# Kernel optimization log

Hardware: AMD Instinct MI355X
Metric: run time of the kernel (lower is better)

Reference implementation:

```python
import jax, jax.numpy as jnp
import numpy as np

B, T, C = 8, 2048, 1024
NEG_BIG = -1e30  # exp(NEG_BIG - row_max) underflows to exactly 0 in fp32


def setup_inputs() -> dict:
    key = jax.random.key(0)
    k1, k2 = jax.random.split(key)
    x = jax.random.normal(k1, (B, T, C), dtype=jnp.float32)
    # nn.Linear weight, shape [out, in]; forward computes x @ W^T
    W_H = jax.random.normal(k2, (C, C), dtype=jnp.float32) * (1.0 / np.sqrt(C))
    return {"x": x, "W_H": W_H}


def reference(x, W_H):
    Tdim = x.shape[1]
    xH = jnp.einsum('btc,dc->btd', x, W_H)          # H(x) = x @ W^T, [B,T,C]
    scores = jnp.einsum('btc,bsc->bts', x, xH)       # bilinear scores, [B,T,T]
    # tril_plus_one=True -> strictly-lower-triangular mask (diagonal=-1)
    mask = jnp.tril(jnp.ones((Tdim, Tdim), dtype=bool), k=-1)
    scores = jnp.where(mask, scores, NEG_BIG)
    wei = jax.nn.softmax(scores, axis=-1)            # fully-masked rows -> uniform, zeroed below
    all_masked = ~mask.any(axis=-1)                  # [T], True for row 0
    wei = jnp.where(all_masked[None, :, None], 0.0, wei)
    out = jnp.einsum('bts,bsc->btc', wei, xH)
    return -out
```

## Files before the change

### kernel.cpp

```cpp
#include <hip/hip_runtime.h>
#include <stdint.h>

#define Bn 8
#define Tn 2048
#define Cn 1024
#define Mn (Bn * Tn)
#define NTRI 136

typedef __attribute__((ext_vector_type(4))) float f32x4;
typedef _Float16 f16;
typedef __attribute__((ext_vector_type(8))) _Float16 f16x8;
typedef uint16_t u16;
typedef uint32_t u32;

static __device__ __forceinline__ u16 f2h(float f) {
  union { f16 h; u16 u; } c; c.h = (f16)f; return c.u;
}
static __device__ __forceinline__ f32x4 mfmaH(f16x8 a, f16x8 b, f32x4 c) {
  return __builtin_amdgcn_mfma_f32_16x16x32_f16(a, b, c, 0, 0, 0);
}
static __device__ __forceinline__ void gld16(const void* g, void* l) {
  __builtin_amdgcn_global_load_lds(
      (const __attribute__((address_space(1))) u32*)g,
      (__attribute__((address_space(3))) u32*)l, 16, 0, 0);
}

__global__ __launch_bounds__(256) void ksplitW(const float* __restrict__ s,
                                               u16* __restrict__ hi) {
  size_t i = ((size_t)blockIdx.x * 256 + threadIdx.x) * 8;
  float4 a = *(const float4*)(s + i), b = *(const float4*)(s + i + 4);
  float f[8] = {a.x, a.y, a.z, a.w, b.x, b.y, b.z, b.w};
  union { u16 u[8]; uint4 v; } H;
#pragma unroll
  for (int j = 0; j < 8; ++j) H.u[j] = f2h(f[j]);
  *(uint4*)(hi + i) = H.v;
}

__global__ __launch_bounds__(256) void ksplitX(const float* __restrict__ s,
                                               u16* __restrict__ hi,
                                               u16* __restrict__ lo) {
  size_t i = ((size_t)blockIdx.x * 256 + threadIdx.x) * 8;
  float4 a = *(const float4*)(s + i), b = *(const float4*)(s + i + 4);
  float f[8] = {a.x, a.y, a.z, a.w, b.x, b.y, b.z, b.w};
  union { u16 u[8]; uint4 v; } H, L;
#pragma unroll
  for (int j = 0; j < 8; ++j) {
    f16 h = (f16)f[j];
    union { f16 h; u16 u; } ch; ch.h = h;
    H.u[j] = ch.u;
    L.u[j] = f2h(f[j] - (float)h);
  }
  *(uint4*)(hi + i) = H.v;
  *(uint4*)(lo + i) = L.v;
}

__global__ __launch_bounds__(256) void k1_xh(const u16* __restrict__ x_h,
                                             const u16* __restrict__ W_h,
                                             u16* __restrict__ xh) {
  __shared__ __align__(16) u16 Ah[8192], Bh[8192];
  const int tid = threadIdx.x;
  const int m0 = blockIdx.x * 128, n0 = blockIdx.y * 128;
  const int wave = tid >> 6, lane = tid & 63;
  const int wrow = (wave >> 1) * 64, wcol = (wave & 1) * 64;
  const int quad = lane >> 4, l16 = lane & 15;

  f32x4 acc[4][4] = {};

  for (int k0 = 0; k0 < Cn; k0 += 64) {
#pragma unroll
    for (int i = 0; i < 4; ++i) {
      int chunk = i * 256 + tid;
      int kk = chunk >> 9, row = (chunk >> 2) & 127, c8 = (chunk & 3) * 8;
      gld16(x_h + (size_t)(m0 + row) * Cn + k0 + kk * 32 + c8, Ah + chunk * 8);
      gld16(W_h + (size_t)(n0 + row) * Cn + k0 + kk * 32 + c8, Bh + chunk * 8);
    }
    __syncthreads();
#pragma unroll
    for (int kk = 0; kk < 2; ++kk) {
      f16x8 a[4], b[4];
#pragma unroll
      for (int i = 0; i < 4; ++i) {
        a[i] = *(const f16x8*)(Ah + kk * 4096 + (wrow + i * 16 + l16) * 32 + quad * 8);
        b[i] = *(const f16x8*)(Bh + kk * 4096 + (wcol + i * 16 + l16) * 32 + quad * 8);
      }
#pragma unroll
      for (int mi = 0; mi < 4; ++mi)
#pragma unroll
        for (int ni = 0; ni < 4; ++ni)
          acc[mi][ni] = mfmaH(a[mi], b[ni], acc[mi][ni]);
    }
    __syncthreads();
  }
#pragma unroll
  for (int mi = 0; mi < 4; ++mi)
#pragma unroll
    for (int ni = 0; ni < 4; ++ni)
#pragma unroll
      for (int r = 0; r < 4; ++r) {
        int row = wrow + mi * 16 + quad * 4 + r;
        int col = wcol + ni * 16 + l16;
        xh[(size_t)(m0 + row) * Cn + n0 + col] = f2h(acc[mi][ni][r]);
      }
}

__global__ __launch_bounds__(512) void k2_scores(const u16* __restrict__ x_h,
                                                 const u16* __restrict__ x_l,
                                                 const u16* __restrict__ xh,
                                                 u16* __restrict__ P,
                                                 float* __restrict__ mt,
                                                 float* __restrict__ lt) {
  __shared__ __align__(16) union {
    struct { u16 Ah[2][4096], Al[2][4096], Bh[2][8192]; } s;
    struct { float Mrow[4][128]; float Lrow[4][128]; } e;
  } u;
  const int tid = threadIdx.x;

  const int bid = blockIdx.x;
  const int half = gridDim.x / 144;
  const int xcd = bid & 7, slot = bid >> 3;
  const int p = xcd & 3, h = xcd >> 2;
  const int n1 = 16 - 2 * p, n2 = 2 * p + 2;
  int c, j, bb;
  if (slot < n1 * half) {
    c = p; bb = slot / n1; j = slot % n1;
  } else {
    int s2 = slot - n1 * half; c = 7 - p; bb = s2 / n2; j = s2 % n2;
  }
  const int bL = h * half + bb;
  const int qt = 2 * c + j, bcol = c;
  const int t0 = qt * 128, s0 = bcol * 256;

  const int wave = tid >> 6, lane = tid & 63;
  const int wc = wave & 3;
  const int wrow = (wave >> 2) * 64, wcol = wc * 64;
  const int quad = lane >> 4, l16 = lane & 15;

  f32x4 acc[4][4] = {};
  const size_t abase = ((size_t)bL * Tn + t0) * Cn;
  const size_t bbase = ((size_t)bL * Tn + s0) * Cn;
  const int arow = tid >> 2, ac8 = (tid & 3) * 8;

  auto stage = [&](int buf, int k0) {
    size_t aoff = abase + (size_t)arow * Cn + k0 + ac8;
    gld16(x_h + aoff, &u.s.Ah[buf][tid * 8]);
    gld16(x_l + aoff, &u.s.Al[buf][tid * 8]);
#pragma unroll
    for (int i = 0; i < 2; ++i) {
      int ch = i * 512 + tid;
      int row = ch >> 2, c8 = (ch & 3) * 8;
      gld16(xh + bbase + (size_t)row * Cn + k0 + c8, &u.s.Bh[buf][ch * 8]);
    }
  };

  stage(0, 0);
  stage(1, 32);
#pragma unroll 1
  for (int kidx = 0; kidx < 32; ++kidx) {
    if (kidx < 31) {
      asm volatile("s_waitcnt vmcnt(4)" ::: "memory");
    } else {
      asm volatile("s_waitcnt vmcnt(0)" ::: "memory");
    }
    __builtin_amdgcn_s_barrier();
    __builtin_amdgcn_sched_barrier(0);
    const int cur = kidx & 1;
    f16x8 b[4];
#pragma unroll
    for (int ni = 0; ni < 4; ++ni)
      b[ni] = *(const f16x8*)&u.s.Bh[cur][(wcol + ni * 16 + l16) * 32 + quad * 8];
#pragma unroll
    for (int mi = 0; mi < 4; ++mi) {
      f16x8 ah = *(const f16x8*)&u.s.Ah[cur][(wrow + mi * 16 + l16) * 32 + quad * 8];
      f16x8 al = *(const f16x8*)&u.s.Al[cur][(wrow + mi * 16 + l16) * 32 + quad * 8];
#pragma unroll
      for (int ni = 0; ni < 4; ++ni) {
        acc[mi][ni] = mfmaH(ah, b[ni], acc[mi][ni]);
        acc[mi][ni] = mfmaH(al, b[ni], acc[mi][ni]);
      }
    }
    asm volatile("s_waitcnt lgkmcnt(0)" ::: "memory");
    __builtin_amdgcn_sched_barrier(0);
    __builtin_amdgcn_s_barrier();
    if (kidx < 30) stage(cur, (kidx + 2) * 32);
  }

  float rm[4][4];
#pragma unroll
  for (int mi = 0; mi < 4; ++mi)
#pragma unroll
    for (int r = 0; r < 4; ++r) {
      int row = wrow + mi * 16 + quad * 4 + r;
      float m = -1e30f;
#pragma unroll
      for (int ni = 0; ni < 4; ++ni) {
        int scol = s0 + wcol + ni * 16 + l16;
        if (scol >= t0 + row) acc[mi][ni][r] = -1e30f;
        m = fmaxf(m, acc[mi][ni][r]);
      }
      m = fmaxf(m, __shfl_xor(m, 1));
      m = fmaxf(m, __shfl_xor(m, 2));
      m = fmaxf(m, __shfl_xor(m, 4));
      m = fmaxf(m, __shfl_xor(m, 8));
      rm[mi][r] = m;
    }
  if (l16 == 0) {
#pragma unroll
    for (int mi = 0; mi < 4; ++mi)
#pragma unroll
      for (int r = 0; r < 4; ++r)
        u.e.Mrow[wc][wrow + mi * 16 + quad * 4 + r] = rm[mi][r];
  }
  __syncthreads();
  const int h2 = (wc >> 1) * 2;
  float rs[4][4];
#pragma unroll
  for (int mi = 0; mi < 4; ++mi)
#pragma unroll
    for (int r = 0; r < 4; ++r) {
      int row = wrow + mi * 16 + quad * 4 + r;
      float m2 = fmaxf(u.e.Mrow[h2][row], u.e.Mrow[h2 + 1][row]);
      float s = 0.f;
#pragma unroll
      for (int ni = 0; ni < 4; ++ni) {
        int scol = s0 + wcol + ni * 16 + l16;
        float pv = (scol < t0 + row) ? __expf(acc[mi][ni][r] - m2) : 0.0f;
        acc[mi][ni][r] = pv;
        s += pv;
      }
      s += __shfl_xor(s, 1);
      s += __shfl_xor(s, 2);
      s += __shfl_xor(s, 4);
      s += __shfl_xor(s, 8);
      rs[mi][r] = s;
      rm[mi][r] = m2;
    }
  if (l16 == 0) {
#pragma unroll
    for (int mi = 0; mi < 4; ++mi)
#pragma unroll
      for (int r = 0; r < 4; ++r)
        u.e.Lrow[wc][wrow + mi * 16 + quad * 4 + r] = rs[mi][r];
  }
  __syncthreads();
  const int st128 = bcol * 2 + (wc >> 1);
  if (st128 <= qt) {
    if ((wc & 1) == 0 && l16 == 0) {
#pragma unroll
      for (int mi = 0; mi < 4; ++mi)
#pragma unroll
        for (int r = 0; r < 4; ++r) {
          int row = wrow + mi * 16 + quad * 4 + r;
          size_t rI = (size_t)bL * Tn + t0 + row;
          mt[rI * 16 + st128] = rm[mi][r];
          lt[rI * 16 + st128] = u.e.Lrow[wc][row] + u.e.Lrow[wc + 1][row];
        }
    }
    const size_t pbase = (size_t)(bL * NTRI + qt * (qt + 1) / 2 + st128) * 16384;
#pragma unroll
    for (int mi = 0; mi < 4; ++mi)
#pragma unroll
      for (int ni = 0; ni < 4; ++ni)
#pragma unroll
        for (int r = 0; r < 4; ++r) {
          int row = wrow + mi * 16 + quad * 4 + r;
          int pcol = (wcol & 64) + ni * 16 + l16;
          P[pbase + row * 128 + pcol] = f2h(acc[mi][ni][r]);
        }
  }
}

__global__ __launch_bounds__(256) void k3_stats(const float* __restrict__ mt,
                                                const float* __restrict__ lt,
                                                float* __restrict__ Mr,
                                                float* __restrict__ Li) {
  int r = blockIdx.x * 256 + threadIdx.x;
  int t = r & (Tn - 1);
  int nt = (t == 0) ? 0 : (((t - 1) >> 7) + 1);
  float M = -1e30f;
  for (int i = 0; i < nt; ++i) M = fmaxf(M, mt[(size_t)r * 16 + i]);
  float L = 0.f;
  for (int i = 0; i < nt; ++i) L += lt[(size_t)r * 16 + i] * __expf(mt[(size_t)r * 16 + i] - M);
  Mr[r] = M;
  Li[r] = (L > 0.f) ? 1.f / L : 0.f;
}

__global__ __launch_bounds__(256) void ktr(const u16* __restrict__ src,
                                           u16* __restrict__ dst) {
  __shared__ __align__(16) u16 S[128 * 136];
  const int t0 = blockIdx.x * 128, c0 = blockIdx.y * 128, b = blockIdx.z;
  const int tid = threadIdx.x;
#pragma unroll
  for (int i = 0; i < 8; ++i) {
    int chunk = tid + i * 256;
    int row = chunk >> 4, c8 = (chunk & 15) * 8;
    uint4 v = *(const uint4*)(src + ((size_t)b * Tn + t0 + row) * Cn + c0 + c8);
    *(uint4*)(S + row * 136 + c8) = v;
  }
  __syncthreads();
#pragma unroll
  for (int i = 0; i < 8; ++i) {
    int chunk = tid + i * 256;
    int crow = chunk >> 4, t8 = (chunk & 15) * 8;
    union { u16 s[8]; uint4 v; } o;
#pragma unroll
    for (int j = 0; j < 8; ++j) o.s[j] = S[(t8 + j) * 136 + crow];
    *(uint4*)(dst + ((size_t)b * Cn + c0 + crow) * Tn + t0 + t8) = o.v;
  }
}

__global__ __launch_bounds__(512) void k4_out(const u16* __restrict__ P,
                                              const u16* __restrict__ xhT,
                                              const float* __restrict__ mt,
                                              const float* __restrict__ Mr,
                                              const float* __restrict__ Li,
                                              float* __restrict__ out) {
  __shared__ __align__(16) u16 Ap[3][4096], Bp[3][8192];
  __shared__ u16 alphaLds[16 * 128];
  const int tid = threadIdx.x;
  const int tt = 15 - blockIdx.x;
  const int cn = blockIdx.y, bL = blockIdx.z;
  const int t0 = tt * 128, c0 = cn * 256;
  const int wave = tid >> 6, lane = tid & 63;
  const int wc = wave & 3;
  const int wrow = (wave >> 2) * 64, wcol = wc * 64;
  const int quad = lane >> 4, l16 = lane & 15;

  {
    const size_t rbase = (size_t)bL * Tn + t0;
#pragma unroll
    for (int j = 0; j < 4; ++j) {
      int idx = tid + j * 512;
      int stp = idx >> 7, row = idx & 127;
      float a = 0.f;
      if (stp <= tt)
        a = __expf(mt[(rbase + row) * 16 + stp] - Mr[rbase + row]) * Li[rbase + row];
      alphaLds[idx] = f2h(a);
    }
  }

  f32x4 acc[4][4] = {};
  const size_t bbase = ((size_t)bL * Cn + c0) * Tn;
  const size_t ptile0 = (size_t)(bL * NTRI + tt * (tt + 1) / 2) * 16384;

  auto stage = [&](int buf, int step) {
    const int st = step >> 2, k32 = (step & 3) * 32;
    {
      int row = tid >> 2, c8 = (tid & 3) * 8;
      gld16(P + ptile0 + (size_t)st * 16384 + row * 128 + k32 + c8,
            &Ap[buf][tid * 8]);
    }
#pragma unroll
    for (int i = 0; i < 2; ++i) {
      int ch = i * 512 + tid;
      int row = ch >> 2, c8 = (ch & 3) * 8;
      gld16(xhT + bbase + (size_t)row * Tn + st * 128 + k32 + c8,
            &Bp[buf][ch * 8]);
    }
  };

  const int steps = 4 * (tt + 1);
  stage(0, 0);
  stage(1, 1);
  int cur = 0;
#pragma unroll 1
  for (int s = 0; s < steps; ++s) {
    if (s < steps - 1) {
      asm volatile("s_waitcnt vmcnt(3) lgkmcnt(0)" ::: "memory");
    } else {
      asm volatile("s_waitcnt vmcnt(0) lgkmcnt(0)" ::: "memory");
    }
    __builtin_amdgcn_s_barrier();
    __builtin_amdgcn_sched_barrier(0);
    if (s < steps - 2) {
      int tgt = cur >= 1 ? cur - 1 : 2;
      stage(tgt, s + 2);
    }
    const int st = s >> 2;
    f16x8 b[4];
#pragma unroll
    for (int ni = 0; ni < 4; ++ni)
      b[ni] = *(const f16x8*)&Bp[cur][(wcol + ni * 16 + l16) * 32 + quad * 8];
#pragma unroll
    for (int mi = 0; mi < 4; ++mi) {
      union { u16 u; f16 h; } ca;
      ca.u = alphaLds[st * 128 + wrow + mi * 16 + l16];
      f16x8 sv;
#pragma unroll
      for (int j = 0; j < 8; ++j) sv[j] = ca.h;
      f16x8 a = *(const f16x8*)&Ap[cur][(wrow + mi * 16 + l16) * 32 + quad * 8];
      a = a * sv;
#pragma unroll
      for (int ni = 0; ni < 4; ++ni)
        acc[mi][ni] = mfmaH(a, b[ni], acc[mi][ni]);
    }
    cur = cur < 2 ? cur + 1 : 0;
  }

#pragma unroll
  for (int mi = 0; mi < 4; ++mi)
#pragma unroll
    for (int ni = 0; ni < 4; ++ni)
#pragma unroll
      for (int r = 0; r < 4; ++r) {
        int row = wrow + mi * 16 + quad * 4 + r;
        int col = wcol + ni * 16 + l16;
        out[((size_t)bL * Tn + t0 + row) * Cn + c0 + col] = -acc[mi][ni][r];
      }
}

extern "C" void kernel_launch(void* const* d_in, const int* in_sizes, int n_in,
                              void* d_out, int out_size, void* d_ws, size_t ws_size,
                              hipStream_t stream) {
  (void)in_sizes; (void)n_in; (void)out_size;
  const float* x = (const float*)d_in[0];
  const float* W = (const float*)d_in[1];
  float* out = (float*)d_out;

  const size_t FULL_NEED = 3ull * Mn * Cn * 2 + (size_t)Bn * NTRI * 16384 * 2 +
                           (size_t)Cn * Cn * 2 + 2ull * Mn * 16 * 4 + 2ull * Mn * 4;
  const int nch = (ws_size >= FULL_NEED) ? 1 : 2;
  const int nb = Bn / nch;
  const size_t rowsC = (size_t)nb * Tn;
  const size_t sA = rowsC * Cn * 2;

  char* p = (char*)d_ws;
  u16* x_h = (u16*)p; p += sA;
  u16* xLT = (u16*)p; p += sA;
  u16* xh  = (u16*)p; p += sA;
  u16* Pp  = (u16*)p; p += (size_t)nb * NTRI * 16384 * 2;
  u16* W_h = (u16*)p; p += (size_t)Cn * Cn * 2;
  float* mt = (float*)p; p += rowsC * 16 * 4;
  float* lt = (float*)p; p += rowsC * 16 * 4;
  float* Mr = (float*)p; p += rowsC * 4;
  float* Li = (float*)p; p += rowsC * 4;

  dim3 blk(256);
  ksplitW<<<dim3(Cn * Cn / 2048), blk, 0, stream>>>(W, W_h);
  for (int c = 0; c < nch; ++c) {
    const float* xc = x + (size_t)c * rowsC * Cn;
    float* oc = out + (size_t)c * rowsC * Cn;
    ksplitX<<<dim3((u32)(rowsC * Cn / 2048)), blk, 0, stream>>>(xc, x_h, xLT);
    k1_xh<<<dim3((u32)(rowsC / 128), Cn / 128), blk, 0, stream>>>(x_h, W_h, xh);
    k2_scores<<<dim3(72 * nb), dim3(512), 0, stream>>>(x_h, xLT, xh, Pp, mt, lt);
    k3_stats<<<dim3((u32)(rowsC / 256)), blk, 0, stream>>>(mt, lt, Mr, Li);
    ktr<<<dim3(Tn / 128, Cn / 128, nb), blk, 0, stream>>>(xh, xLT);
    k4_out<<<dim3(16, Cn / 256, nb), dim3(512), 0, stream>>>(Pp, xLT, mt, Mr, Li, oc);
  }
}
```

Measured before the change: 385.9 us.

## XOR-swizzle LDS tiles and triple-buffer the scores kernel pipeline

Global-to-LDS loads now place each 16-byte chunk at an XOR-swizzled column, and the MFMA operand reads apply the matching swizzle, in the xH, scores and output GEMM kernels. The goal is to cut LDS bank conflicts on the 32-element-wide rows. The scores kernel also moves from double to triple buffering and issues the next stage right after the barrier, which drops the second barrier per k-step. This raises LDS use in that kernel, which may lower occupancy.

```diff
diff --git a/kernel.cpp b/kernel.cpp
--- a/kernel.cpp
+++ b/kernel.cpp
@@ -24,6 +24,7 @@
       (const __attribute__((address_space(1))) u32*)g,
       (__attribute__((address_space(3))) u32*)l, 16, 0, 0);
 }
+
 
 __global__ __launch_bounds__(256) void ksplitW(const float* __restrict__ s,
                                                u16* __restrict__ hi) {
@@ -63,6 +64,8 @@
   const int wave = tid >> 6, lane = tid & 63;
   const int wrow = (wave >> 1) * 64, wcol = (wave & 1) * 64;
   const int quad = lane >> 4, l16 = lane & 15;
+  const int ssw = ((((tid >> 3) & 3) ^ (tid & 3))) * 8;
+  const int qs8 = (quad ^ ((l16 >> 1) & 3)) * 8;
 
   f32x4 acc[4][4] = {};
 
@@ -70,9 +73,9 @@
 #pragma unroll
     for (int i = 0; i < 4; ++i) {
       int chunk = i * 256 + tid;
-      int kk = chunk >> 9, row = (chunk >> 2) & 127, c8 = (chunk & 3) * 8;
-      gld16(x_h + (size_t)(m0 + row) * Cn + k0 + kk * 32 + c8, Ah + chunk * 8);
-      gld16(W_h + (size_t)(n0 + row) * Cn + k0 + kk * 32 + c8, Bh + chunk * 8);
+      int kk = chunk >> 9, row = (chunk >> 2) & 127;
+      gld16(x_h + (size_t)(m0 + row) * Cn + k0 + kk * 32 + ssw, Ah + chunk * 8);
+      gld16(W_h + (size_t)(n0 + row) * Cn + k0 + kk * 32 + ssw, Bh + chunk * 8);
     }
     __syncthreads();
 #pragma unroll
@@ -80,8 +83,8 @@
       f16x8 a[4], b[4];
 #pragma unroll
       for (int i = 0; i < 4; ++i) {
-        a[i] = *(const f16x8*)(Ah + kk * 4096 + (wrow + i * 16 + l16) * 32 + quad * 8);
-        b[i] = *(const f16x8*)(Bh + kk * 4096 + (wcol + i * 16 + l16) * 32 + quad * 8);
+        a[i] = *(const f16x8*)(Ah + kk * 4096 + (wrow + i * 16 + l16) * 32 + qs8);
+        b[i] = *(const f16x8*)(Bh + kk * 4096 + (wcol + i * 16 + l16) * 32 + qs8);
       }
 #pragma unroll
       for (int mi = 0; mi < 4; ++mi)
@@ -110,7 +113,7 @@
                                                  float* __restrict__ mt,
                                                  float* __restrict__ lt) {
   __shared__ __align__(16) union {
-    struct { u16 Ah[2][4096], Al[2][4096], Bh[2][8192]; } s;
+    struct { u16 Ah[3][4096], Al[3][4096], Bh[3][8192]; } s;
     struct { float Mrow[4][128]; float Lrow[4][128]; } e;
   } u;
   const int tid = threadIdx.x;
@@ -134,54 +137,57 @@
   const int wc = wave & 3;
   const int wrow = (wave >> 2) * 64, wcol = wc * 64;
   const int quad = lane >> 4, l16 = lane & 15;
+  const int ssw = ((((tid >> 3) & 3) ^ (tid & 3))) * 8;
+  const int qs8 = (quad ^ ((l16 >> 1) & 3)) * 8;
 
   f32x4 acc[4][4] = {};
   const size_t abase = ((size_t)bL * Tn + t0) * Cn;
   const size_t bbase = ((size_t)bL * Tn + s0) * Cn;
-  const int arow = tid >> 2, ac8 = (tid & 3) * 8;
+  const int arow = tid >> 2;
 
   auto stage = [&](int buf, int k0) {
-    size_t aoff = abase + (size_t)arow * Cn + k0 + ac8;
+    size_t aoff = abase + (size_t)arow * Cn + k0 + ssw;
     gld16(x_h + aoff, &u.s.Ah[buf][tid * 8]);
     gld16(x_l + aoff, &u.s.Al[buf][tid * 8]);
 #pragma unroll
     for (int i = 0; i < 2; ++i) {
       int ch = i * 512 + tid;
-      int row = ch >> 2, c8 = (ch & 3) * 8;
-      gld16(xh + bbase + (size_t)row * Cn + k0 + c8, &u.s.Bh[buf][ch * 8]);
+      int row = ch >> 2;
+      gld16(xh + bbase + (size_t)row * Cn + k0 + ssw, &u.s.Bh[buf][ch * 8]);
     }
   };
 
   stage(0, 0);
   stage(1, 32);
+  int cur = 0;
 #pragma unroll 1
   for (int kidx = 0; kidx < 32; ++kidx) {
     if (kidx < 31) {
-      asm volatile("s_waitcnt vmcnt(4)" ::: "memory");
+      asm volatile("s_waitcnt vmcnt(4) lgkmcnt(0)" ::: "memory");
     } else {
-      asm volatile("s_waitcnt vmcnt(0)" ::: "memory");
+      asm volatile("s_waitcnt vmcnt(0) lgkmcnt(0)" ::: "memory");
     }
     __builtin_amdgcn_s_barrier();
     __builtin_amdgcn_sched_barrier(0);
-    const int cur = kidx & 1;
+    if (kidx < 30) {
+      int tgt = cur >= 1 ? cur - 1 : 2;
+      stage(tgt, (kidx + 2) * 32);
+    }
     f16x8 b[4];
 #pragma unroll
     for (int ni = 0; ni < 4; ++ni)
-      b[ni] = *(const f16x8*)&u.s.Bh[cur][(wcol + ni * 16 + l16) * 32 + quad * 8];
+      b[ni] = *(const f16x8*)&u.s.Bh[cur][(wcol + ni * 16 + l16) * 32 + qs8];
 #pragma unroll
     for (int mi = 0; mi < 4; ++mi) {
-      f16x8 ah = *(const f16x8*)&u.s.Ah[cur][(wrow + mi * 16 + l16) * 32 + quad * 8];
-      f16x8 al = *(const f16x8*)&u.s.Al[cur][(wrow + mi * 16 + l16) * 32 + quad * 8];
+      f16x8 ah = *(const f16x8*)&u.s.Ah[cur][(wrow + mi * 16 + l16) * 32 + qs8];
+      f16x8 al = *(const f16x8*)&u.s.Al[cur][(wrow + mi * 16 + l16) * 32 + qs8];
 #pragma unroll
       for (int ni = 0; ni < 4; ++ni) {
         acc[mi][ni] = mfmaH(ah, b[ni], acc[mi][ni]);
         acc[mi][ni] = mfmaH(al, b[ni], acc[mi][ni]);
       }
     }
-    asm volatile("s_waitcnt lgkmcnt(0)" ::: "memory");
-    __builtin_amdgcn_sched_barrier(0);
-    __builtin_amdgcn_s_barrier();
-    if (kidx < 30) stage(cur, (kidx + 2) * 32);
+    cur = cur < 2 ? cur + 1 : 0;
   }
 
   float rm[4][4];
@@ -324,6 +330,8 @@
   const int wc = wave & 3;
   const int wrow = (wave >> 2) * 64, wcol = wc * 64;
   const int quad = lane >> 4, l16 = lane & 15;
+  const int ssw = ((((tid >> 3) & 3) ^ (tid & 3))) * 8;
+  const int qs8 = (quad ^ ((l16 >> 1) & 3)) * 8;
 
   {
     const size_t rbase = (size_t)bL * Tn + t0;
@@ -345,15 +353,15 @@
   auto stage = [&](int buf, int step) {
     const int st = step >> 2, k32 = (step & 3) * 32;
     {
-      int row = tid >> 2, c8 = (tid & 3) * 8;
-      gld16(P + ptile0 + (size_t)st * 16384 + row * 128 + k32 + c8,
+      int row = tid >> 2;
+      gld16(P + ptile0 + (size_t)st * 16384 + row * 128 + k32 + ssw,
             &Ap[buf][tid * 8]);
     }
 #pragma unroll
     for (int i = 0; i < 2; ++i) {
       int ch = i * 512 + tid;
-      int row = ch >> 2, c8 = (ch & 3) * 8;
-      gld16(xhT + bbase + (size_t)row * Tn + st * 128 + k32 + c8,
+      int row = ch >> 2;
+      gld16(xhT + bbase + (size_t)row * Tn + st * 128 + k32 + ssw,
             &Bp[buf][ch * 8]);
     }
   };
@@ -379,7 +387,7 @@
     f16x8 b[4];
 #pragma unroll
     for (int ni = 0; ni < 4; ++ni)
-      b[ni] = *(const f16x8*)&Bp[cur][(wcol + ni * 16 + l16) * 32 + quad * 8];
+      b[ni] = *(const f16x8*)&Bp[cur][(wcol + ni * 16 + l16) * 32 + qs8];
 #pragma unroll
     for (int mi = 0; mi < 4; ++mi) {
       union { u16 u; f16 h; } ca;
@@ -387,7 +395,7 @@
       f16x8 sv;
 #pragma unroll
       for (int j = 0; j < 8; ++j) sv[j] = ca.h;
-      f16x8 a = *(const f16x8*)&Ap[cur][(wrow + mi * 16 + l16) * 32 + quad * 8];
+      f16x8 a = *(const f16x8*)&Ap[cur][(wrow + mi * 16 + l16) * 32 + qs8];
       a = a * sv;
 #pragma unroll
       for (int ni = 0; ni < 4; ++ni)
```

Measured after the change: 365.9 us. -5.2%, faster.
